# Optimization experiments

Measured on AMD Instinct MI355X. Metric: run time of the kernel, lower is better.

Reference implementation:

```python
import jax, jax.numpy as jnp
import numpy as np
import math

EMB_DIM = 2048
HEAD_NUMS = 16
HEAD_DIM = EMB_DIM // HEAD_NUMS


def setup_inputs() -> dict:
    key = jax.random.key(0)
    k1, k2, k3, k4, k5 = jax.random.split(key, 5)
    B, S = 2, 2048
    X = jax.random.normal(k1, (B, S, EMB_DIM), dtype=jnp.float32)
    mask = jnp.ones((B, S), dtype=jnp.int32)
    # torch nn.Linear weights: [out_features, in_features]
    W_qkv = jax.random.normal(k2, (3 * EMB_DIM, EMB_DIM), dtype=jnp.float32) / math.sqrt(EMB_DIM)
    b_qkv = jax.random.normal(k3, (3 * EMB_DIM,), dtype=jnp.float32) * 0.01
    W_o = jax.random.normal(k4, (EMB_DIM, EMB_DIM), dtype=jnp.float32) / math.sqrt(EMB_DIM)
    b_o = jax.random.normal(k5, (EMB_DIM,), dtype=jnp.float32) * 0.01
    return {"X": X, "mask": mask, "W_qkv": W_qkv, "b_qkv": b_qkv, "W_o": W_o, "b_o": b_o}


def _rope_tables(seq_len):
    # Bug-faithful to source: exponent divides by full emb_dim, not head_dim.
    angle = 1.0 / jnp.power(10000.0, jnp.arange(0, HEAD_DIM, 2, dtype=jnp.float32) / EMB_DIM)
    t = jnp.arange(seq_len, dtype=jnp.float32)
    freqs = t[:, None] * angle[None, :]            # [S, HEAD_DIM//2]
    freqs = jnp.repeat(freqs, 2, axis=-1)          # [S, HEAD_DIM] (repeat_interleave)
    return jnp.cos(freqs), jnp.sin(freqs)


def _trans(x):
    # de-interleave pairs, then concat([-odd, even]) along last dim (as in source)
    B, H, S, D = x.shape
    xr = x.reshape(B, H, S, D // 2, 2)
    x1, x2 = xr[..., 0], xr[..., 1]
    return jnp.concatenate([-x2, x1], axis=-1)


def reference(X, mask, W_qkv, b_qkv, W_o, b_o):
    B, S, E = X.shape
    cos, sin = _rope_tables(S)                      # [S, HEAD_DIM]
    qkv = X @ W_qkv.T + b_qkv                       # [B, S, 3E]
    qkv = qkv.reshape(B, S, 3, HEAD_NUMS, HEAD_DIM).transpose(2, 0, 3, 1, 4)
    Q, K, V = qkv[0], qkv[1], qkv[2]                # [B, H, S, D]
    c = cos[None, None, :, :]
    s = sin[None, None, :, :]
    Q = c * Q + s * _trans(Q)
    K = c * K + s * _trans(K)
    scores = jnp.einsum('bhqd,bhkd->bhqk', Q, K) / math.sqrt(HEAD_DIM)
    pad = mask[:, None, None, :]                    # [B,1,1,S]
    scores = jnp.where(pad == 0, -1e9, scores)
    attn = jax.nn.softmax(scores, axis=-1)          # dropout = identity (eval)
    out = jnp.einsum('bhqk,bhkd->bhqd', attn, V)    # [B,H,S,D]
    out = out.transpose(0, 2, 1, 3).reshape(B, S, E)
    return out @ W_o.T + b_o
```

## Files before the change

### kernel.cpp

```cpp
#include <hip/hip_runtime.h>
#include <hip/hip_bf16.h>
#include <math.h>

typedef __bf16 bf16x8 __attribute__((ext_vector_type(8)));
typedef float  f32x4  __attribute__((ext_vector_type(4)));
typedef float  f32x16 __attribute__((ext_vector_type(16)));
typedef unsigned short ushort_t;
typedef ushort_t us4 __attribute__((ext_vector_type(4)));

#define MFMA16(a, b, c) __builtin_amdgcn_mfma_f32_16x16x32_bf16((a), (b), (c), 0, 0, 0)
#define MFMA32(a, b, c) __builtin_amdgcn_mfma_f32_32x32x16_bf16((a), (b), (c), 0, 0, 0)

__device__ __forceinline__ float bf2f(ushort_t h) {
    union { unsigned u; float f; } v; v.u = ((unsigned)h) << 16; return v.f;
}
__device__ __forceinline__ ushort_t f2bf(float x) {
    union { float f; unsigned u; } v; v.f = x;
    unsigned r = v.u + 0x7FFFu + ((v.u >> 16) & 1u);
    return (ushort_t)(r >> 16);
}
__device__ __forceinline__ void gl2lds16(const void* g, void* l) {
    __builtin_amdgcn_global_load_lds((__attribute__((address_space(1))) void*)(g),
                                     (__attribute__((address_space(3))) void*)(l),
                                     16, 0, 0);
}

__global__ __launch_bounds__(256) void detect_kernel(const ushort_t* __restrict__ w, int* flag)
{
    __shared__ int cnt[256];
    const int t = threadIdx.x;
    int c = 0;
    for (int i = t; i < 65536; i += 256) {
        const unsigned hw = w[i];
        const unsigned e = (hw >> 7) & 0xFFu;
        if (e == 0xFFu || (e == 0u && (hw & 0x7Fu) != 0u)) c++;
    }
    cnt[t] = c;
    __syncthreads();
    for (int s = 128; s > 0; s >>= 1) {
        if (t < s) cnt[t] += cnt[t + s];
        __syncthreads();
    }
    if (t == 0) flag[0] = (cnt[0] >= 8) ? 1 : 0;
}

__global__ __launch_bounds__(256) void convert_kernel(const void* __restrict__ src,
                                                      ushort_t* __restrict__ dst,
                                                      int n, const int* __restrict__ flag)
{
    const int i0 = (blockIdx.x * 256 + threadIdx.x) * 8;
    if (i0 + 8 > n) return;
    if (flag[0]) {
        const f32x4 a = *(const f32x4*)((const float*)src + i0);
        const f32x4 b = *(const f32x4*)((const float*)src + i0 + 4);
        ushort_t o[8];
        o[0]=f2bf(a[0]); o[1]=f2bf(a[1]); o[2]=f2bf(a[2]); o[3]=f2bf(a[3]);
        o[4]=f2bf(b[0]); o[5]=f2bf(b[1]); o[6]=f2bf(b[2]); o[7]=f2bf(b[3]);
        *(bf16x8*)(dst + i0) = *(const bf16x8*)o;
    } else {
        *(bf16x8*)(dst + i0) = *(const bf16x8*)((const ushort_t*)src + i0);
    }
}

__global__ __launch_bounds__(512, 2) void gemm256_bt_bias(
    const ushort_t* __restrict__ A, const ushort_t* __restrict__ B,
    const ushort_t* __restrict__ bias, ushort_t* __restrict__ C,
    int M, int N, int K)
{
    __shared__ __align__(16) ushort_t SM[65536];
    const int tid = threadIdx.x;
    const int l = tid & 63, ln = l & 15, q2 = l >> 4;
    const int w = tid >> 6, wm = w >> 2, wn = w & 3;
    const int m0 = blockIdx.y * 256, n0 = blockIdx.x * 256;
    const int NT = K >> 6;

#define STG_A256(slot, kbase, o) do { \
    const int s_ = (o) * 512 + tid; const int r_ = s_ >> 2; \
    const int q_ = (s_ & 3) ^ ((r_ >> 1) & 3); \
    gl2lds16(A + (size_t)(m0 + r_) * K + (kbase) + q_ * 8, \
             SM + (slot) * 16384 + s_ * 8); } while (0)
#define STG_B256(slot, kbase, o) do { \
    const int s_ = (o) * 512 + tid; const int r_ = s_ >> 2; \
    const int q_ = (s_ & 3) ^ ((r_ >> 1) & 3); \
    gl2lds16(B + (size_t)(n0 + r_) * K + (kbase) + q_ * 8, \
             SM + (slot) * 16384 + 8192 + s_ * 8); } while (0)
#define DSA256(slot, row) (*(const bf16x8*)(SM + (slot) * 16384 + (row) * 32 + ((q2 ^ (((row) >> 1) & 3)) << 3)))
#define DSB256(slot, row) (*(const bf16x8*)(SM + (slot) * 16384 + 8192 + (row) * 32 + ((q2 ^ (((row) >> 1) & 3)) << 3)))
#define BAR256() asm volatile("s_barrier" ::: "memory")

    f32x4 acc[8][4];
    const f32x4 z4 = {0.f, 0.f, 0.f, 0.f};
#pragma unroll
    for (int i = 0; i < 8; i++)
#pragma unroll
        for (int j = 0; j < 4; j++) acc[i][j] = z4;

    STG_A256(0, 0, 0);  STG_A256(0, 0, 1);  STG_B256(0, 0, 0);  STG_B256(0, 0, 1);
    STG_A256(1, 32, 0); STG_A256(1, 32, 1); STG_B256(1, 32, 0); STG_B256(1, 32, 1);
    asm volatile("s_waitcnt vmcnt(4)" ::: "memory");
    BAR256();

    for (int t = 0; t < NT; ++t) {
        const int s0 = (2 * t) & 3, s1 = (2 * t + 1) & 3;
        const int sA = (2 * t + 2) & 3, sB = (2 * t + 3) & 3;
        const int kA = (t + 1) << 6, kB = kA + 32;
        const bool stAB = (t < NT - 1);
        const int rA0 = wm * 128, rA1 = wm * 128 + 64, rB = wn * 64;
        bf16x8 a[4], b0[4], b1[4];

#pragma unroll
        for (int ii = 0; ii < 4; ii++) a[ii]  = DSA256(s0, rA0 + ii * 16 + ln);
#pragma unroll
        for (int jj = 0; jj < 4; jj++) b0[jj] = DSB256(s0, rB + jj * 16 + ln);
        if (stAB) { STG_A256(sA, kA, 0); STG_A256(sA, kA, 1); }
        __builtin_amdgcn_s_setprio(1);
#pragma unroll
        for (int ii = 0; ii < 4; ii++)
#pragma unroll
            for (int jj = 0; jj < 4; jj++)
                acc[ii][jj] = MFMA16(a[ii], b0[jj], acc[ii][jj]);
        __builtin_amdgcn_s_setprio(0);
        if (stAB) { asm volatile("s_waitcnt vmcnt(2)" ::: "memory"); }
        else      { asm volatile("s_waitcnt vmcnt(0)" ::: "memory"); }
        BAR256();

#pragma unroll
        for (int ii = 0; ii < 4; ii++) a[ii]  = DSA256(s1, rA0 + ii * 16 + ln);
#pragma unroll
        for (int jj = 0; jj < 4; jj++) b1[jj] = DSB256(s1, rB + jj * 16 + ln);
        if (stAB) { STG_B256(sA, kA, 0); STG_B256(sA, kA, 1); }
        __builtin_amdgcn_s_setprio(1);
#pragma unroll
        for (int ii = 0; ii < 4; ii++)
#pragma unroll
            for (int jj = 0; jj < 4; jj++)
                acc[ii][jj] = MFMA16(a[ii], b1[jj], acc[ii][jj]);
        __builtin_amdgcn_s_setprio(0);
        BAR256();

#pragma unroll
        for (int ii = 0; ii < 4; ii++) a[ii] = DSA256(s0, rA1 + ii * 16 + ln);
        if (stAB) { STG_A256(sB, kB, 0); STG_A256(sB, kB, 1); }
        __builtin_amdgcn_s_setprio(1);
#pragma unroll
        for (int ii = 0; ii < 4; ii++)
#pragma unroll
            for (int jj = 0; jj < 4; jj++)
                acc[4 + ii][jj] = MFMA16(a[ii], b0[jj], acc[4 + ii][jj]);
        __builtin_amdgcn_s_setprio(0);
        BAR256();

#pragma unroll
        for (int ii = 0; ii < 4; ii++) a[ii] = DSA256(s1, rA1 + ii * 16 + ln);
        if (stAB) { STG_B256(sB, kB, 0); STG_B256(sB, kB, 1); }
        __builtin_amdgcn_s_setprio(1);
#pragma unroll
        for (int ii = 0; ii < 4; ii++)
#pragma unroll
            for (int jj = 0; jj < 4; jj++)
                acc[4 + ii][jj] = MFMA16(a[ii], b1[jj], acc[4 + ii][jj]);
        __builtin_amdgcn_s_setprio(0);
        if (stAB) { asm volatile("s_waitcnt vmcnt(4)" ::: "memory"); }
        BAR256();
    }

#pragma unroll
    for (int j = 0; j < 4; j++) {
        const int n = n0 + wn * 64 + j * 16 + ln;
        const float bv = bf2f(bias[n]);
#pragma unroll
        for (int i = 0; i < 8; i++) {
            const int mrow = m0 + wm * 128 + i * 16 + q2 * 4;
#pragma unroll
            for (int r = 0; r < 4; r++)
                C[(size_t)(mrow + r) * N + n] = f2bf(acc[i][j][r] + bv);
        }
    }
#undef STG_A256
#undef STG_B256
#undef DSA256
#undef DSB256
#undef BAR256
}

__global__ __launch_bounds__(256) void gemm_bt_bias_out(
    const ushort_t* __restrict__ A, const ushort_t* __restrict__ B,
    const ushort_t* __restrict__ bias, void* __restrict__ C,
    int M, int N, int K, const int* __restrict__ flag)
{
    __shared__ __align__(16) ushort_t As[128 * 32];
    __shared__ __align__(16) ushort_t Bs[128 * 32];
    const int tid = threadIdx.x;
    const int w = tid >> 6, l = tid & 63, q = l >> 4, ln = l & 15;
    const int wm = w >> 1, wn = w & 1;
    const int m0 = blockIdx.y * 128, n0 = blockIdx.x * 128;
    const int sr = tid >> 2;
    const int sc = (tid & 3) * 8;

    f32x4 acc[4][4];
    const f32x4 z4 = {0.f, 0.f, 0.f, 0.f};
    for (int i = 0; i < 4; i++) for (int j = 0; j < 4; j++) acc[i][j] = z4;

    for (int k0 = 0; k0 < K; k0 += 32) {
        __syncthreads();
        gl2lds16(A + (size_t)(m0 + sr) * K + k0 + sc,       As + sr * 32 + sc);
        gl2lds16(A + (size_t)(m0 + 64 + sr) * K + k0 + sc,  As + (64 + sr) * 32 + sc);
        gl2lds16(B + (size_t)(n0 + sr) * K + k0 + sc,       Bs + sr * 32 + sc);
        gl2lds16(B + (size_t)(n0 + 64 + sr) * K + k0 + sc,  Bs + (64 + sr) * 32 + sc);
        __syncthreads();
        bf16x8 a[4], bb[4];
        for (int i = 0; i < 4; i++)
            a[i]  = *(const bf16x8*)(As + (wm * 64 + i * 16 + ln) * 32 + q * 8);
        for (int j = 0; j < 4; j++)
            bb[j] = *(const bf16x8*)(Bs + (wn * 64 + j * 16 + ln) * 32 + q * 8);
        for (int i = 0; i < 4; i++)
            for (int j = 0; j < 4; j++)
                acc[i][j] = MFMA16(a[i], bb[j], acc[i][j]);
    }
    const int f = flag[0];
    for (int j = 0; j < 4; j++) {
        const int n = n0 + wn * 64 + j * 16 + ln;
        const float bv = bf2f(bias[n]);
        for (int i = 0; i < 4; i++) {
            const int mrow = m0 + wm * 64 + i * 16 + q * 4;
            for (int r = 0; r < 4; r++) {
                const float val = acc[i][j][r] + bv;
                const size_t idx = (size_t)(mrow + r) * N + n;
                if (f) ((float*)C)[idx] = val;
                else   ((ushort_t*)C)[idx] = f2bf(val);
            }
        }
    }
}

__global__ __launch_bounds__(256) void rope_kernel(ushort_t* qkv)
{
    const int bs = blockIdx.x;
    const int s = bs & 2047;
    const int t = threadIdx.x;
    const size_t base = (size_t)bs * 6144;
    float cv[8], sv[8], qa[8], qp[8], ka[8], kp[8];
    for (int u = 0; u < 8; u++) {
        const int e = u * 256 + t;
        const int j = e & 127;
        const int p = (j < 64) ? (2 * j + 1) : (2 * (j - 64));
        const int hb = e - j;
        const float ang = powf(10000.0f, -(float)(2 * (j >> 1)) / 2048.0f);
        sincosf((float)s * ang, &sv[u], &cv[u]);
        qa[u] = bf2f(qkv[base + hb + j]);
        qp[u] = bf2f(qkv[base + hb + p]);
        ka[u] = bf2f(qkv[base + 2048 + hb + j]);
        kp[u] = bf2f(qkv[base + 2048 + hb + p]);
    }
    __syncthreads();
    for (int u = 0; u < 8; u++) {
        const int e = u * 256 + t;
        const int j = e & 127;
        const int hb = e - j;
        const float sg = (j < 64) ? -1.0f : 1.0f;
        qkv[base + hb + j]        = f2bf(cv[u] * qa[u] + sv[u] * sg * qp[u]);
        qkv[base + 2048 + hb + j] = f2bf(cv[u] * ka[u] + sv[u] * sg * kp[u]);
    }
}

__global__ __launch_bounds__(256) void vtrans_kernel(const ushort_t* __restrict__ qkv,
                                                     ushort_t* __restrict__ Vt)
{
    __shared__ ushort_t tile[64][130];
    const int blk = blockIdx.x;
    const int st = blk & 31, h = (blk >> 5) & 15, b = blk >> 9;
    const int t = threadIdx.x;
    for (int i = 0; i < 32; i++) {
        const int e = i * 256 + t;
        const int r = e >> 7, c = e & 127;
        tile[r][c] = qkv[(size_t)(b * 2048 + st * 64 + r) * 6144 + 4096 + h * 128 + c];
    }
    __syncthreads();
    const int d = t >> 1, s0 = (t & 1) * 32;
    const size_t obase = ((size_t)(b * 16 + h) * 128 + d) * 2048 + st * 64 + s0;
    for (int k = 0; k < 32; k++)
        Vt[obase + k] = tile[s0 + k][d];
}

__global__ __launch_bounds__(256, 2) void flash_kernel(
    const ushort_t* __restrict__ qkv, const ushort_t* __restrict__ Vt,
    const int* __restrict__ mask, ushort_t* __restrict__ AO)
{
    __shared__ __align__(16) ushort_t SM[16384];
    ushort_t* Ks = SM;
    ushort_t* Vs = SM + 8192;
    const int t = threadIdx.x;
    const int w = t >> 6, l = t & 63, lq = l & 31, q2 = l >> 5;
    const int qb = blockIdx.x * 128, h = blockIdx.y, b = blockIdx.z;
    const size_t brow = (size_t)b * 2048;
    const float scale = 0.08838834764831845f;
    const int qrow = qb + w * 32 + lq;
    const size_t vbase = (size_t)(b * 16 + h) * 128;

    bf16x8 qf[8];
#pragma unroll
    for (int kb = 0; kb < 8; kb++)
        qf[kb] = *(const bf16x8*)(qkv + (brow + qrow) * 6144 + h * 128 + kb * 16 + q2 * 8);

    float m_old = -1e30f, lsum = 0.f;
    f32x16 acc_o[4];
#pragma unroll
    for (int dt = 0; dt < 4; dt++)
#pragma unroll
        for (int r = 0; r < 16; r++) acc_o[dt][r] = 0.f;

    bf16x8 kst[4], vst[4];
#pragma unroll
    for (int i = 0; i < 4; i++) {
        const int s_ = i * 256 + t; const int row = s_ >> 4; const int u = s_ & 15;
        kst[i] = *(const bf16x8*)(qkv + (brow + row) * 6144 + 2048 + h * 128 + u * 8);
    }
#pragma unroll
    for (int i = 0; i < 4; i++) {
        const int s_ = i * 256 + t; const int row = s_ >> 3; const int u = s_ & 7;
        vst[i] = *(const bf16x8*)(Vt + (vbase + row) * 2048 + u * 8);
    }

    for (int s0 = 0; s0 < 2048; s0 += 64) {
        const int mk = mask[brow + s0 + l];
        const unsigned long long bm = __ballot(mk != 0);
        asm volatile("s_waitcnt lgkmcnt(0)" ::: "memory");
        asm volatile("s_barrier" ::: "memory");
#pragma unroll
        for (int i = 0; i < 4; i++) {
            const int s_ = i * 256 + t; const int row = s_ >> 4; const int u = s_ & 15;
            *(bf16x8*)(Ks + row * 128 + ((u ^ (row & 15)) << 3)) = kst[i];
        }
#pragma unroll
        for (int i = 0; i < 4; i++) {
            const int s_ = i * 256 + t; const int row = s_ >> 3; const int u = s_ & 7;
            *(bf16x8*)(Vs + row * 64 + ((u ^ (row & 7)) << 3)) = vst[i];
        }
        if (s0 + 64 < 2048) {
#pragma unroll
            for (int i = 0; i < 4; i++) {
                const int s_ = i * 256 + t; const int row = s_ >> 4; const int u = s_ & 15;
                kst[i] = *(const bf16x8*)(qkv + (brow + s0 + 64 + row) * 6144 + 2048 + h * 128 + u * 8);
            }
#pragma unroll
            for (int i = 0; i < 4; i++) {
                const int s_ = i * 256 + t; const int row = s_ >> 3; const int u = s_ & 7;
                vst[i] = *(const bf16x8*)(Vt + (vbase + row) * 2048 + s0 + 64 + u * 8);
            }
        }
        asm volatile("s_waitcnt lgkmcnt(0)" ::: "memory");
        asm volatile("s_barrier" ::: "memory");

        f32x16 sa[2];
#pragma unroll
        for (int mt = 0; mt < 2; mt++) {
#pragma unroll
            for (int r = 0; r < 16; r++) sa[mt][r] = 0.f;
            const int row = mt * 32 + lq;
            __builtin_amdgcn_s_setprio(1);
#pragma unroll
            for (int kb = 0; kb < 8; kb++) {
                bf16x8 a = *(const bf16x8*)(Ks + row * 128 + (((kb * 2 + q2) ^ (row & 15)) << 3));
                sa[mt] = MFMA32(a, qf[kb], sa[mt]);
            }
            __builtin_amdgcn_s_setprio(0);
        }
        float p[32];
        float mr = -1e30f;
        if (bm == ~0ull) {
#pragma unroll
            for (int mt = 0; mt < 2; mt++)
#pragma unroll
                for (int r = 0; r < 16; r++) {
                    const float v = sa[mt][r] * scale;
                    p[mt * 16 + r] = v;
                    mr = fmaxf(mr, v);
                }
        } else {
#pragma unroll
            for (int mt = 0; mt < 2; mt++)
#pragma unroll
                for (int r = 0; r < 16; r++) {
                    const int srow = mt * 32 + (r & 3) + 8 * (r >> 2) + 4 * q2;
                    const float bias = ((bm >> srow) & 1ull) ? 0.f : -1e9f;
                    const float v = sa[mt][r] * scale + bias;
                    p[mt * 16 + r] = v;
                    mr = fmaxf(mr, v);
                }
        }
        mr = fmaxf(mr, __shfl_xor(mr, 32, 64));
        if (!__all(mr <= m_old + 8.0f)) {
            const float mnew = fmaxf(m_old, mr);
            const float alpha = __expf(m_old - mnew);
            lsum *= alpha;
#pragma unroll
            for (int dt = 0; dt < 4; dt++)
#pragma unroll
                for (int r = 0; r < 16; r++) acc_o[dt][r] *= alpha;
            m_old = mnew;
        }
        float rs = 0.f;
#pragma unroll
        for (int i = 0; i < 32; i++) { p[i] = __expf(p[i] - m_old); rs += p[i]; }
        rs += __shfl_xor(rs, 32, 64);
        lsum += rs;

#pragma unroll
        for (int kb = 0; kb < 4; kb++) {
            const int bb = (kb >> 1) * 16 + (kb & 1) * 8;
            unsigned w01, w23, w45, w67;
            asm("v_cvt_pk_bf16_f32 %0, %1, %2" : "=v"(w01) : "v"(p[bb + 0]), "v"(p[bb + 1]));
            asm("v_cvt_pk_bf16_f32 %0, %1, %2" : "=v"(w23) : "v"(p[bb + 2]), "v"(p[bb + 3]));
            asm("v_cvt_pk_bf16_f32 %0, %1, %2" : "=v"(w45) : "v"(p[bb + 4]), "v"(p[bb + 5]));
            asm("v_cvt_pk_bf16_f32 %0, %1, %2" : "=v"(w67) : "v"(p[bb + 6]), "v"(p[bb + 7]));
            asm("v_permlane32_swap_b32 %0, %1" : "+v"(w01), "+v"(w45));
            asm("v_permlane32_swap_b32 %0, %1" : "+v"(w23), "+v"(w67));
            union { unsigned u[4]; bf16x8 v8; } pu;
            pu.u[0] = w01; pu.u[1] = w23; pu.u[2] = w45; pu.u[3] = w67;
            __builtin_amdgcn_s_setprio(1);
#pragma unroll
            for (int dt = 0; dt < 4; dt++) {
                const int row = dt * 32 + lq;
                bf16x8 va = *(const bf16x8*)(Vs + row * 64 + (((kb * 2 + q2) ^ (row & 7)) << 3));
                acc_o[dt] = MFMA32(va, pu.v8, acc_o[dt]);
            }
            __builtin_amdgcn_s_setprio(0);
        }
    }
    __syncthreads();
    const float inv = (lsum > 0.f) ? 1.0f / lsum : 0.f;
#pragma unroll
    for (int dt = 0; dt < 4; dt++)
#pragma unroll
        for (int r2 = 0; r2 < 4; r2++) {
            us4 ov;
#pragma unroll
            for (int j = 0; j < 4; j++) ov[j] = f2bf(acc_o[dt][r2 * 4 + j] * inv);
            const int row = w * 32 + lq;
            const int unit = dt * 4 + r2;
            *(us4*)(SM + row * 128 + ((unit ^ (row & 15)) << 3) + q2 * 4) = ov;
        }
    __syncthreads();
#pragma unroll
    for (int i = 0; i < 8; i++) {
        const int rl = i * 4 + (l >> 4), ch = l & 15;
        const int row = w * 32 + rl;
        bf16x8 vv = *(const bf16x8*)(SM + row * 128 + ((ch ^ (row & 15)) << 3));
        *(bf16x8*)(AO + (brow + qb + row) * 2048 + h * 128 + ch * 8) = vv;
    }
}

extern "C" void kernel_launch(void* const* d_in, const int* in_sizes, int n_in,
                              void* d_out, int out_size, void* d_ws, size_t ws_size,
                              hipStream_t stream)
{
    (void)in_sizes; (void)n_in; (void)out_size; (void)ws_size;
    const void* X    = d_in[0];
    const int*  mask = (const int*)d_in[1];
    const void* Wqkv = d_in[2];
    const void* bqkv = d_in[3];
    const void* Wo   = d_in[4];
    const void* bo   = d_in[5];

    int*      flag  = (int*)d_ws;
    ushort_t* Xc    = (ushort_t*)d_ws + 16;
    ushort_t* Wqkvc = Xc + 8388608;
    ushort_t* bqkvc = Wqkvc + 12582912;
    ushort_t* Woc   = bqkvc + 6144;
    ushort_t* boc   = Woc + 4194304;
    ushort_t* qkv   = boc + 2048;
    ushort_t* Vt    = Wqkvc;
    ushort_t* AO    = Xc;

    detect_kernel<<<1, 256, 0, stream>>>((const ushort_t*)Wqkv, flag);
    convert_kernel<<<4096, 256, 0, stream>>>(X,    Xc,    8388608,  flag);
    convert_kernel<<<6144, 256, 0, stream>>>(Wqkv, Wqkvc, 12582912, flag);
    convert_kernel<<<3,    256, 0, stream>>>(bqkv, bqkvc, 6144,     flag);
    convert_kernel<<<2048, 256, 0, stream>>>(Wo,   Woc,   4194304,  flag);
    convert_kernel<<<1,    256, 0, stream>>>(bo,   boc,   2048,     flag);

    gemm256_bt_bias<<<dim3(6144 / 256, 4096 / 256), 512, 0, stream>>>(Xc, Wqkvc, bqkvc, qkv, 4096, 6144, 2048);
    rope_kernel<<<4096, 256, 0, stream>>>(qkv);
    vtrans_kernel<<<1024, 256, 0, stream>>>(qkv, Vt);
    flash_kernel<<<dim3(16, 16, 2), 256, 0, stream>>>(qkv, Vt, mask, AO);
    gemm_bt_bias_out<<<dim3(2048 / 128, 4096 / 128), 256, 0, stream>>>(AO, Woc, boc, d_out, 4096, 2048, 2048, flag);
}
```

Measured before the change: 579.0 us.

## Software-pipeline LDS fragment loads with MFMAs and deepen global prefetch

```diff
diff --git a/kernel.cpp b/kernel.cpp
--- a/kernel.cpp
+++ b/kernel.cpp
@@ -95,72 +95,85 @@
 #pragma unroll
         for (int j = 0; j < 4; j++) acc[i][j] = z4;
 
+    const int rA0 = wm * 128, rA1 = wm * 128 + 64, rB = wn * 64;
+
     STG_A256(0, 0, 0);  STG_A256(0, 0, 1);  STG_B256(0, 0, 0);  STG_B256(0, 0, 1);
     STG_A256(1, 32, 0); STG_A256(1, 32, 1); STG_B256(1, 32, 0); STG_B256(1, 32, 1);
-    asm volatile("s_waitcnt vmcnt(4)" ::: "memory");
+    STG_A256(2, 64, 0); STG_A256(2, 64, 1);
+    asm volatile("s_waitcnt vmcnt(2)" ::: "memory");
     BAR256();
+
+    bf16x8 a[4], b0[4], b1[4];
+#pragma unroll
+    for (int ii = 0; ii < 4; ii++) a[ii]  = DSA256(0, rA0 + ii * 16 + ln);
+#pragma unroll
+    for (int jj = 0; jj < 4; jj++) b0[jj] = DSB256(0, rB + jj * 16 + ln);
 
     for (int t = 0; t < NT; ++t) {
         const int s0 = (2 * t) & 3, s1 = (2 * t + 1) & 3;
-        const int sA = (2 * t + 2) & 3, sB = (2 * t + 3) & 3;
-        const int kA = (t + 1) << 6, kB = kA + 32;
-        const bool stAB = (t < NT - 1);
-        const int rA0 = wm * 128, rA1 = wm * 128 + 64, rB = wn * 64;
-        bf16x8 a[4], b0[4], b1[4];
-
-#pragma unroll
-        for (int ii = 0; ii < 4; ii++) a[ii]  = DSA256(s0, rA0 + ii * 16 + ln);
-#pragma unroll
-        for (int jj = 0; jj < 4; jj++) b0[jj] = DSB256(s0, rB + jj * 16 + ln);
-        if (stAB) { STG_A256(sA, kA, 0); STG_A256(sA, kA, 1); }
+        const int sA2 = (2 * t + 2) & 3, sB2 = (2 * t + 3) & 3;
+        const int kA2 = (t + 1) << 6, kB2 = kA2 + 32, kC = (t + 2) << 6;
+        const bool stAB = (t < NT - 1), stC = (t < NT - 2);
+
+        if (stAB) { STG_B256(sA2, kA2, 0); STG_B256(sA2, kA2, 1); }
+#pragma unroll
+        for (int jj = 0; jj < 4; jj++) b1[jj] = DSB256(s1, rB + jj * 16 + ln);
         __builtin_amdgcn_s_setprio(1);
 #pragma unroll
-        for (int ii = 0; ii < 4; ii++)
-#pragma unroll
-            for (int jj = 0; jj < 4; jj++)
-                acc[ii][jj] = MFMA16(a[ii], b0[jj], acc[ii][jj]);
-        __builtin_amdgcn_s_setprio(0);
-        if (stAB) { asm volatile("s_waitcnt vmcnt(2)" ::: "memory"); }
-        else      { asm volatile("s_waitcnt vmcnt(0)" ::: "memory"); }
-        BAR256();
-
-#pragma unroll
-        for (int ii = 0; ii < 4; ii++) a[ii]  = DSA256(s1, rA0 + ii * 16 + ln);
-#pragma unroll
-        for (int jj = 0; jj < 4; jj++) b1[jj] = DSB256(s1, rB + jj * 16 + ln);
-        if (stAB) { STG_B256(sA, kA, 0); STG_B256(sA, kA, 1); }
-        __builtin_amdgcn_s_setprio(1);
-#pragma unroll
-        for (int ii = 0; ii < 4; ii++)
-#pragma unroll
-            for (int jj = 0; jj < 4; jj++)
-                acc[ii][jj] = MFMA16(a[ii], b1[jj], acc[ii][jj]);
+        for (int ii = 0; ii < 4; ii++) {
+            acc[ii][0] = MFMA16(a[ii], b0[0], acc[ii][0]);
+            acc[ii][1] = MFMA16(a[ii], b0[1], acc[ii][1]);
+            acc[ii][2] = MFMA16(a[ii], b0[2], acc[ii][2]);
+            acc[ii][3] = MFMA16(a[ii], b0[3], acc[ii][3]);
+            a[ii] = DSA256(s1, rA0 + ii * 16 + ln);
+        }
         __builtin_amdgcn_s_setprio(0);
         BAR256();
 
-#pragma unroll
-        for (int ii = 0; ii < 4; ii++) a[ii] = DSA256(s0, rA1 + ii * 16 + ln);
-        if (stAB) { STG_A256(sB, kB, 0); STG_A256(sB, kB, 1); }
+        if (stAB) { STG_A256(sB2, kB2, 0); STG_A256(sB2, kB2, 1); }
         __builtin_amdgcn_s_setprio(1);
 #pragma unroll
-        for (int ii = 0; ii < 4; ii++)
-#pragma unroll
-            for (int jj = 0; jj < 4; jj++)
-                acc[4 + ii][jj] = MFMA16(a[ii], b0[jj], acc[4 + ii][jj]);
+        for (int ii = 0; ii < 4; ii++) {
+            acc[ii][0] = MFMA16(a[ii], b1[0], acc[ii][0]);
+            acc[ii][1] = MFMA16(a[ii], b1[1], acc[ii][1]);
+            acc[ii][2] = MFMA16(a[ii], b1[2], acc[ii][2]);
+            acc[ii][3] = MFMA16(a[ii], b1[3], acc[ii][3]);
+            a[ii] = DSA256(s0, rA1 + ii * 16 + ln);
+        }
         __builtin_amdgcn_s_setprio(0);
         BAR256();
 
-#pragma unroll
-        for (int ii = 0; ii < 4; ii++) a[ii] = DSA256(s1, rA1 + ii * 16 + ln);
-        if (stAB) { STG_B256(sB, kB, 0); STG_B256(sB, kB, 1); }
+        if (stAB) { STG_B256(sB2, kB2, 0); STG_B256(sB2, kB2, 1); }
         __builtin_amdgcn_s_setprio(1);
 #pragma unroll
-        for (int ii = 0; ii < 4; ii++)
-#pragma unroll
-            for (int jj = 0; jj < 4; jj++)
-                acc[4 + ii][jj] = MFMA16(a[ii], b1[jj], acc[4 + ii][jj]);
+        for (int ii = 0; ii < 4; ii++) {
+            acc[4 + ii][0] = MFMA16(a[ii], b0[0], acc[4 + ii][0]);
+            acc[4 + ii][1] = MFMA16(a[ii], b0[1], acc[4 + ii][1]);
+            acc[4 + ii][2] = MFMA16(a[ii], b0[2], acc[4 + ii][2]);
+            acc[4 + ii][3] = MFMA16(a[ii], b0[3], acc[4 + ii][3]);
+            a[ii] = DSA256(s1, rA1 + ii * 16 + ln);
+        }
         __builtin_amdgcn_s_setprio(0);
         if (stAB) { asm volatile("s_waitcnt vmcnt(4)" ::: "memory"); }
+        BAR256();
+
+        if (stC) { STG_A256(s0, kC, 0); STG_A256(s0, kC, 1); }
+        if (stAB) {
+#pragma unroll
+            for (int jj = 0; jj < 4; jj++) b0[jj] = DSB256(sA2, rB + jj * 16 + ln);
+        }
+        __builtin_amdgcn_s_setprio(1);
+#pragma unroll
+        for (int ii = 0; ii < 4; ii++) {
+            acc[4 + ii][0] = MFMA16(a[ii], b1[0], acc[4 + ii][0]);
+            acc[4 + ii][1] = MFMA16(a[ii], b1[1], acc[4 + ii][1]);
+            acc[4 + ii][2] = MFMA16(a[ii], b1[2], acc[4 + ii][2]);
+            acc[4 + ii][3] = MFMA16(a[ii], b1[3], acc[4 + ii][3]);
+            if (stAB) a[ii] = DSA256(sA2, rA0 + ii * 16 + ln);
+        }
+        __builtin_amdgcn_s_setprio(0);
+        if (stC)             { asm volatile("s_waitcnt vmcnt(2)" ::: "memory"); }
+        else if (t == NT - 2){ asm volatile("s_waitcnt vmcnt(0)" ::: "memory"); }
         BAR256();
     }
 
```

Result: no change. 583.3 us (+0.8%).

## Replace 256x256 QKV GEMM with 128x128 tiles and triple-buffered LDS pipeline

Applied to the files above, without the earlier changes.

```diff
diff --git a/kernel.cpp b/kernel.cpp
--- a/kernel.cpp
+++ b/kernel.cpp
@@ -62,106 +62,67 @@
     }
 }
 
-__global__ __launch_bounds__(512, 2) void gemm256_bt_bias(
+__global__ __launch_bounds__(256, 3) void gemm_qkv_bt_bias(
     const ushort_t* __restrict__ A, const ushort_t* __restrict__ B,
     const ushort_t* __restrict__ bias, ushort_t* __restrict__ C,
     int M, int N, int K)
 {
-    __shared__ __align__(16) ushort_t SM[65536];
+    __shared__ __align__(16) ushort_t SM[24576];
     const int tid = threadIdx.x;
     const int l = tid & 63, ln = l & 15, q2 = l >> 4;
-    const int w = tid >> 6, wm = w >> 2, wn = w & 3;
-    const int m0 = blockIdx.y * 256, n0 = blockIdx.x * 256;
-    const int NT = K >> 6;
-
-#define STG_A256(slot, kbase, o) do { \
-    const int s_ = (o) * 512 + tid; const int r_ = s_ >> 2; \
+    const int w = tid >> 6, wm = w >> 1, wn = w & 1;
+    const int m0 = blockIdx.y * 128, n0 = blockIdx.x * 128;
+    const int NC = K >> 5;
+
+#define STG_A(slot, kbase, o) do { \
+    const int s_ = (o) * 256 + tid; const int r_ = s_ >> 2; \
     const int q_ = (s_ & 3) ^ ((r_ >> 1) & 3); \
     gl2lds16(A + (size_t)(m0 + r_) * K + (kbase) + q_ * 8, \
-             SM + (slot) * 16384 + s_ * 8); } while (0)
-#define STG_B256(slot, kbase, o) do { \
-    const int s_ = (o) * 512 + tid; const int r_ = s_ >> 2; \
+             SM + (slot) * 8192 + s_ * 8); } while (0)
+#define STG_B(slot, kbase, o) do { \
+    const int s_ = (o) * 256 + tid; const int r_ = s_ >> 2; \
     const int q_ = (s_ & 3) ^ ((r_ >> 1) & 3); \
     gl2lds16(B + (size_t)(n0 + r_) * K + (kbase) + q_ * 8, \
-             SM + (slot) * 16384 + 8192 + s_ * 8); } while (0)
-#define DSA256(slot, row) (*(const bf16x8*)(SM + (slot) * 16384 + (row) * 32 + ((q2 ^ (((row) >> 1) & 3)) << 3)))
-#define DSB256(slot, row) (*(const bf16x8*)(SM + (slot) * 16384 + 8192 + (row) * 32 + ((q2 ^ (((row) >> 1) & 3)) << 3)))
-#define BAR256() asm volatile("s_barrier" ::: "memory")
-
-    f32x4 acc[8][4];
+             SM + (slot) * 8192 + 4096 + s_ * 8); } while (0)
+#define DSA(slot, row) (*(const bf16x8*)(SM + (slot) * 8192 + (row) * 32 + ((q2 ^ (((row) >> 1) & 3)) << 3)))
+#define DSB(slot, row) (*(const bf16x8*)(SM + (slot) * 8192 + 4096 + (row) * 32 + ((q2 ^ (((row) >> 1) & 3)) << 3)))
+#define BARQ() asm volatile("s_barrier" ::: "memory")
+
+    f32x4 acc[4][4];
     const f32x4 z4 = {0.f, 0.f, 0.f, 0.f};
 #pragma unroll
-    for (int i = 0; i < 8; i++)
+    for (int i = 0; i < 4; i++)
 #pragma unroll
         for (int j = 0; j < 4; j++) acc[i][j] = z4;
 
-    STG_A256(0, 0, 0);  STG_A256(0, 0, 1);  STG_B256(0, 0, 0);  STG_B256(0, 0, 1);
-    STG_A256(1, 32, 0); STG_A256(1, 32, 1); STG_B256(1, 32, 0); STG_B256(1, 32, 1);
+    STG_A(0, 0, 0);  STG_A(0, 0, 1);  STG_B(0, 0, 0);  STG_B(0, 0, 1);
+    STG_A(1, 32, 0); STG_A(1, 32, 1); STG_B(1, 32, 0); STG_B(1, 32, 1);
     asm volatile("s_waitcnt vmcnt(4)" ::: "memory");
-    BAR256();
-
-    for (int t = 0; t < NT; ++t) {
-        const int s0 = (2 * t) & 3, s1 = (2 * t + 1) & 3;
-        const int sA = (2 * t + 2) & 3, sB = (2 * t + 3) & 3;
-        const int kA = (t + 1) << 6, kB = kA + 32;
-        const bool stAB = (t < NT - 1);
-        const int rA0 = wm * 128, rA1 = wm * 128 + 64, rB = wn * 64;
-        bf16x8 a[4], b0[4], b1[4];
-
-#pragma unroll
-        for (int ii = 0; ii < 4; ii++) a[ii]  = DSA256(s0, rA0 + ii * 16 + ln);
-#pragma unroll
-        for (int jj = 0; jj < 4; jj++) b0[jj] = DSB256(s0, rB + jj * 16 + ln);
-        if (stAB) { STG_A256(sA, kA, 0); STG_A256(sA, kA, 1); }
+    BARQ();
+
+    int scur = 0;
+    for (int c = 0; c < NC; ++c) {
+        const int s2 = (scur >= 1) ? scur - 1 : scur + 2;
+        if (c <= NC - 3) {
+            const int kn = (c + 2) << 5;
+            STG_A(s2, kn, 0); STG_A(s2, kn, 1); STG_B(s2, kn, 0); STG_B(s2, kn, 1);
+        }
+        bf16x8 a[4], b[4];
+#pragma unroll
+        for (int ii = 0; ii < 4; ii++) a[ii] = DSA(scur, wm * 64 + ii * 16 + ln);
+#pragma unroll
+        for (int jj = 0; jj < 4; jj++) b[jj] = DSB(scur, wn * 64 + jj * 16 + ln);
         __builtin_amdgcn_s_setprio(1);
 #pragma unroll
         for (int ii = 0; ii < 4; ii++)
 #pragma unroll
             for (int jj = 0; jj < 4; jj++)
-                acc[ii][jj] = MFMA16(a[ii], b0[jj], acc[ii][jj]);
+                acc[ii][jj] = MFMA16(a[ii], b[jj], acc[ii][jj]);
         __builtin_amdgcn_s_setprio(0);
-        if (stAB) { asm volatile("s_waitcnt vmcnt(2)" ::: "memory"); }
-        else      { asm volatile("s_waitcnt vmcnt(0)" ::: "memory"); }
-        BAR256();
-
-#pragma unroll
-        for (int ii = 0; ii < 4; ii++) a[ii]  = DSA256(s1, rA0 + ii * 16 + ln);
-#pragma unroll
-        for (int jj = 0; jj < 4; jj++) b1[jj] = DSB256(s1, rB + jj * 16 + ln);
-        if (stAB) { STG_B256(sA, kA, 0); STG_B256(sA, kA, 1); }
-        __builtin_amdgcn_s_setprio(1);
-#pragma unroll
-        for (int ii = 0; ii < 4; ii++)
-#pragma unroll
-            for (int jj = 0; jj < 4; jj++)
-                acc[ii][jj] = MFMA16(a[ii], b1[jj], acc[ii][jj]);
-        __builtin_amdgcn_s_setprio(0);
-        BAR256();
-
-#pragma unroll
-        for (int ii = 0; ii < 4; ii++) a[ii] = DSA256(s0, rA1 + ii * 16 + ln);
-        if (stAB) { STG_A256(sB, kB, 0); STG_A256(sB, kB, 1); }
-        __builtin_amdgcn_s_setprio(1);
-#pragma unroll
-        for (int ii = 0; ii < 4; ii++)
-#pragma unroll
-            for (int jj = 0; jj < 4; jj++)
-                acc[4 + ii][jj] = MFMA16(a[ii], b0[jj], acc[4 + ii][jj]);
-        __builtin_amdgcn_s_setprio(0);
-        BAR256();
-
-#pragma unroll
-        for (int ii = 0; ii < 4; ii++) a[ii] = DSA256(s1, rA1 + ii * 16 + ln);
-        if (stAB) { STG_B256(sB, kB, 0); STG_B256(sB, kB, 1); }
-        __builtin_amdgcn_s_setprio(1);
-#pragma unroll
-        for (int ii = 0; ii < 4; ii++)
-#pragma unroll
-            for (int jj = 0; jj < 4; jj++)
-                acc[4 + ii][jj] = MFMA16(a[ii], b1[jj], acc[4 + ii][jj]);
-        __builtin_amdgcn_s_setprio(0);
-        if (stAB) { asm volatile("s_waitcnt vmcnt(4)" ::: "memory"); }
-        BAR256();
+        if (c <= NC - 3)      { asm volatile("s_waitcnt vmcnt(4)" ::: "memory"); }
+        else if (c == NC - 2) { asm volatile("s_waitcnt vmcnt(0)" ::: "memory"); }
+        BARQ();
+        scur = (scur == 2) ? 0 : scur + 1;
     }
 
 #pragma unroll
@@ -169,18 +130,18 @@
         const int n = n0 + wn * 64 + j * 16 + ln;
         const float bv = bf2f(bias[n]);
 #pragma unroll
-        for (int i = 0; i < 8; i++) {
-            const int mrow = m0 + wm * 128 + i * 16 + q2 * 4;
+        for (int i = 0; i < 4; i++) {
+            const int mrow = m0 + wm * 64 + i * 16 + q2 * 4;
 #pragma unroll
             for (int r = 0; r < 4; r++)
                 C[(size_t)(mrow + r) * N + n] = f2bf(acc[i][j][r] + bv);
         }
     }
-#undef STG_A256
-#undef STG_B256
-#undef DSA256
-#undef DSB256
-#undef BAR256
+#undef STG_A
+#undef STG_B
+#undef DSA
+#undef DSB
+#undef BARQ
 }
 
 __global__ __launch_bounds__(256) void gemm_bt_bias_out(
@@ -479,7 +440,7 @@
     convert_kernel<<<2048, 256, 0, stream>>>(Wo,   Woc,   4194304,  flag);
     convert_kernel<<<1,    256, 0, stream>>>(bo,   boc,   2048,     flag);
 
-    gemm256_bt_bias<<<dim3(6144 / 256, 4096 / 256), 512, 0, stream>>>(Xc, Wqkvc, bqkvc, qkv, 4096, 6144, 2048);
+    gemm_qkv_bt_bias<<<dim3(6144 / 128, 4096 / 128), 256, 0, stream>>>(Xc, Wqkvc, bqkvc, qkv, 4096, 6144, 2048);
     rope_kernel<<<4096, 256, 0, stream>>>(qkv);
     vtrans_kernel<<<1024, 256, 0, stream>>>(qkv, Vt);
     flash_kernel<<<dim3(16, 16, 2), 256, 0, stream>>>(qkv, Vt, mask, AO);
```

New measurement: 616.4 us. 1.06x slower.
